# Kernel optimization log

Measured on AMD Instinct MI355X. Metric: run time of the kernel, lower is better.

Reference implementation:

```python
import jax, jax.numpy as jnp
import numpy as np

RANGE_EXTENDER = 5.0
EPS = 1e-8  # torch cosine_similarity eps

N_CLASSES = 256
LATENT = 256
H = W = 256


def setup_inputs() -> dict:
    key = jax.random.key(0)
    k1, k2, k3 = jax.random.split(key, 3)
    x = jax.random.normal(k1, (LATENT, H, W), dtype=jnp.float32)
    weights = jax.random.normal(k2, (N_CLASSES, LATENT), dtype=jnp.float32)
    scale = jax.random.normal(k3, (N_CLASSES,), dtype=jnp.float32)
    return {"x": x, "weights": weights, "scale": scale}


def reference(x, weights, scale):
    # out[c,i,j] = cos_sim(x[:,i,j], weights[c]) * scale[c] * RANGE_EXTENDER
    x_norm = jnp.sqrt(jnp.sum(x * x, axis=0, keepdims=True))           # (1, H, W)
    xn = x / jnp.maximum(x_norm, EPS)                                   # (D, H, W)
    w_norm = jnp.sqrt(jnp.sum(weights * weights, axis=1, keepdims=True))  # (C, 1)
    wn = weights / jnp.maximum(w_norm, EPS)                             # (C, D)
    cos = jnp.einsum("cd,dhw->chw", wn, xn)                            # (C, H, W)
    return cos * scale[:, None, None] * RANGE_EXTENDER
```

## Files before the change

kernel.cpp:

```cpp
#include <hip/hip_runtime.h>
#include <stdint.h>

typedef unsigned short u16;
typedef __bf16 bf16_t;
typedef bf16_t bf16x8 __attribute__((ext_vector_type(8)));
typedef float f32x4 __attribute__((ext_vector_type(4)));

static constexpr int P = 65536;

__device__ __forceinline__ float bfbits2f(uint32_t b) {
    union { uint32_t i; float f; } u; u.i = b << 16; return u.f;
}
__device__ __forceinline__ u16 f2bf(float f) {
    union { float f; uint32_t i; } u; u.f = f;
    uint32_t x = u.i + 0x7FFFu + ((u.i >> 16) & 1u);
    return (u16)(x >> 16);
}
__device__ __forceinline__ uint32_t pack2(float a, float b) {
    return (uint32_t)f2bf(a) | ((uint32_t)f2bf(b) << 16);
}

__device__ __forceinline__ int detect_bf16_input(const void* Xg) {
    const uint32_t* Xu = (const uint32_t*)Xg;
    const int lane = (int)(threadIdx.x & 63);
    const uint32_t v = Xu[(size_t)lane * 131071u];
    const uint32_t e = (v >> 7) & 0xFFu;
    unsigned long long m = __ballot(e >= 96u && e <= 135u);
    return __popcll(m) >= 40;
}

__global__ __launch_bounds__(64) void coshead_prep(
    const void* __restrict__ Xg, const void* __restrict__ Wg,
    const void* __restrict__ Sg, float* __restrict__ rs_ws,
    u16* __restrict__ wbf)
{
    const int c    = (int)blockIdx.x;
    const int lane = (int)threadIdx.x;
    const int bf   = detect_bf16_input(Xg);
    float s;
    uint2 packed;
    if (bf) {
        const uint2 v = *(const uint2*)((const u16*)Wg + (size_t)c * 256 + lane * 4);
        const float a = bfbits2f(v.x & 0xFFFFu), b = bfbits2f(v.x >> 16);
        const float d = bfbits2f(v.y & 0xFFFFu), e = bfbits2f(v.y >> 16);
        s = a * a + b * b + d * d + e * e;
        packed = v;
    } else {
        const f32x4 v = *(const f32x4*)((const float*)Wg + (size_t)c * 256 + lane * 4);
        s = v[0] * v[0] + v[1] * v[1] + v[2] * v[2] + v[3] * v[3];
        packed.x = pack2(v[0], v[1]);
        packed.y = pack2(v[2], v[3]);
    }
    *(uint2*)(wbf + (size_t)c * 256 + lane * 4) = packed;
    s += __shfl_xor(s, 1);  s += __shfl_xor(s, 2);  s += __shfl_xor(s, 4);
    s += __shfl_xor(s, 8);  s += __shfl_xor(s, 16); s += __shfl_xor(s, 32);
    if (lane == 0) {
        const float sc = bf ? bfbits2f((uint32_t)((const u16*)Sg)[c])
                            : ((const float*)Sg)[c];
        rs_ws[c] = sc * 5.0f / fmaxf(sqrtf(s), 1e-8f);
    }
}

__global__ __launch_bounds__(256, 3) void coshead_gemm(
    const void* __restrict__ Xg_, const u16* __restrict__ Wbf,
    const float* __restrict__ rs_ws, float* __restrict__ Og)
{
    __shared__ char smem_[32768 + 8192];
    char* sA = smem_;
    char* sB = smem_ + 32768;

    const int t  = (int)threadIdx.x;
    const int l  = t & 63;
    const int w  = t >> 6;
    const int p0 = (int)blockIdx.x * 64;
    const int bf = detect_bf16_input(Xg_);

    const int g    = t & 7;
    const int r    = t >> 3;
    const int m16  = l & 15;
    const int quad = l >> 4;

    const int lrow = l >> 3;
    const int gsl  = (l & 7) ^ lrow;
    const u16* wsrc = Wbf + ((size_t)(w * 8 + lrow) << 8) + gsl * 8;
    char* ldsA = sA + w * 1024;

    float ssq[8];
#pragma unroll
    for (int j = 0; j < 8; ++j) ssq[j] = 0.f;
    f32x4 acc[4][4];
#pragma unroll
    for (int a = 0; a < 4; ++a)
#pragma unroll
        for (int b = 0; b < 4; ++b)
#pragma unroll
            for (int i = 0; i < 4; ++i) acc[a][b][i] = 0.f;

    f32x4 rA, rB, rC, rD;
    if (!bf) {
        const float* xp = (const float*)Xg_ + (size_t)(2 * r) * P + p0 + g * 8;
        rA = *(const f32x4*)xp;
        rB = *(const f32x4*)(xp + 4);
        rC = *(const f32x4*)(xp + P);
        rD = *(const f32x4*)(xp + P + 4);
    }

    for (int kc = 0; kc < 4; ++kc) {
#pragma unroll
        for (int j = 0; j < 8; ++j) {
            __builtin_amdgcn_global_load_lds(
                (const __attribute__((address_space(1))) void*)(wsrc + j * 8192 + kc * 64),
                (__attribute__((address_space(3))) void*)(ldsA + j * 4096),
                16, 0, 0);
        }

        if (bf) {
            const u16* xp = (const u16*)Xg_ + (size_t)(2 * r + kc * 64) * P + p0 + g * 8;
            const uint4 v0 = *(const uint4*)xp;
            const uint4 v1 = *(const uint4*)(xp + P);
            const uint32_t e0[4] = {v0.x, v0.y, v0.z, v0.w};
            const uint32_t e1[4] = {v1.x, v1.y, v1.z, v1.w};
#pragma unroll
            for (int d = 0; d < 4; ++d) {
                const float f00 = bfbits2f(e0[d] & 0xFFFFu), f01 = bfbits2f(e0[d] >> 16);
                const float f10 = bfbits2f(e1[d] & 0xFFFFu), f11 = bfbits2f(e1[d] >> 16);
                ssq[2 * d]     += f00 * f00 + f10 * f10;
                ssq[2 * d + 1] += f01 * f01 + f11 * f11;
                const uint32_t d0 = (e0[d] & 0xFFFFu) | (e1[d] << 16);
                const uint32_t d1 = (e0[d] >> 16) | (e1[d] & 0xFFFF0000u);
                const int pj0 = g * 8 + 2 * d, pj1 = pj0 + 1;
                *(uint32_t*)(sB + pj0 * 128 + (((r >> 2) ^ (pj0 & 7) ^ g) * 16) + (r & 3) * 4) = d0;
                *(uint32_t*)(sB + pj1 * 128 + (((r >> 2) ^ (pj1 & 7) ^ g) * 16) + (r & 3) * 4) = d1;
            }
        } else {
            const float f0[8] = {rA[0], rA[1], rA[2], rA[3], rB[0], rB[1], rB[2], rB[3]};
            const float f1[8] = {rC[0], rC[1], rC[2], rC[3], rD[0], rD[1], rD[2], rD[3]};
#pragma unroll
            for (int j = 0; j < 8; ++j) {
                ssq[j] += f0[j] * f0[j] + f1[j] * f1[j];
                const int pix = g * 8 + j;
                *(uint32_t*)(sB + pix * 128 + (((r >> 2) ^ (pix & 7) ^ g) * 16) + (r & 3) * 4) =
                    pack2(f0[j], f1[j]);
            }
        }
        __syncthreads();

        if (!bf && kc < 3) {
            const float* xp = (const float*)Xg_ + (size_t)(2 * r + (kc + 1) * 64) * P + p0 + g * 8;
            rA = *(const f32x4*)xp;
            rB = *(const f32x4*)(xp + 4);
            rC = *(const f32x4*)(xp + P);
            rD = *(const f32x4*)(xp + P + 4);
        }

#pragma unroll
        for (int kk = 0; kk < 2; ++kk) {
            bf16x8 af[4], bfr[4];
#pragma unroll
            for (int tm = 0; tm < 4; ++tm) {
                const int row = w * 64 + tm * 16 + m16;
                af[tm] = *(const bf16x8*)(sA + row * 128 + (((kk * 4 + quad) ^ (row & 7)) * 16));
            }
#pragma unroll
            for (int tn = 0; tn < 4; ++tn) {
                const int pix = tn * 16 + m16;
                bfr[tn] = *(const bf16x8*)(sB + pix * 128 +
                           (((kk * 4 + quad) ^ (pix & 7) ^ (pix >> 3)) * 16));
            }
#pragma unroll
            for (int tm = 0; tm < 4; ++tm)
#pragma unroll
                for (int tn = 0; tn < 4; ++tn)
                    acc[tm][tn] = __builtin_amdgcn_mfma_f32_16x16x32_bf16(
                        af[tm], bfr[tn], acc[tm][tn], 0, 0, 0);
        }
        __syncthreads();
    }

    float* xs   = (float*)sA;
    float* xinv = (float*)sB;
#pragma unroll
    for (int j = 0; j < 8; ++j) xs[r * 64 + g * 8 + j] = ssq[j];
    __syncthreads();
    if (t < 64) {
        float sx = 0.f;
#pragma unroll
        for (int rr = 0; rr < 32; ++rr) sx += xs[rr * 64 + t];
        xinv[t] = 1.0f / fmaxf(sqrtf(sx), 1e-8f);
    }
    __syncthreads();

    float inv4[4];
#pragma unroll
    for (int tn = 0; tn < 4; ++tn) inv4[tn] = xinv[tn * 16 + m16];
#pragma unroll
    for (int tm = 0; tm < 4; ++tm) {
        const int cbase = w * 64 + tm * 16 + quad * 4;
        const f32x4 rs4 = *(const f32x4*)(rs_ws + cbase);
#pragma unroll
        for (int tn = 0; tn < 4; ++tn) {
#pragma unroll
            for (int i = 0; i < 4; ++i) {
                Og[(size_t)(cbase + i) * P + p0 + tn * 16 + m16] =
                    acc[tm][tn][i] * rs4[i] * inv4[tn];
            }
        }
    }
}

extern "C" void kernel_launch(void* const* d_in, const int* in_sizes, int n_in,
                              void* d_out, int out_size, void* d_ws, size_t ws_size,
                              hipStream_t stream) {
    (void)out_size; (void)ws_size;
    const void* X = d_in[0];
    const void* W = d_in[1];
    const void* S = d_in[2];
    for (int i = 0; i < n_in; ++i) {
        if (in_sizes[i] == 256 * 65536) X = d_in[i];
        else if (in_sizes[i] == 256 * 256) W = d_in[i];
        else if (in_sizes[i] == 256)      S = d_in[i];
    }
    float* rs  = (float*)d_ws;
    u16*   wbf = (u16*)((char*)d_ws + 1024);
    coshead_prep<<<dim3(256), dim3(64), 0, stream>>>(X, W, S, rs, wbf);
    coshead_gemm<<<dim3(1024), dim3(256), 0, stream>>>(X, wbf, rs, (float*)d_out);
}
```

Measured before the change: 139.6 us.

## Keep full weight matrix resident in LDS and loop four pixel tiles per block

The GEMM kernel now loads the whole bf16 weight matrix (128 KB) into LDS once per block and reuses it across four 64-pixel tiles. The grid shrinks from 1024 to 256 blocks. The B tile is double-buffered, so one barrier per k-step replaces two, and the next X chunk is prefetched across tile boundaries. This cuts repeated weight traffic and per-block setup, at the cost of one block per CU (occupancy 1, launch bounds 256,1) with a 256-block grid, which may leave CUs idle or underused on a 256-CU part and loses latency hiding.

Result: faster. 131.6 us (-5.7%).

```diff
diff --git a/kernel.cpp b/kernel.cpp
--- a/kernel.cpp
+++ b/kernel.cpp
@@ -61,18 +61,19 @@
     }
 }
 
-__global__ __launch_bounds__(256, 3) void coshead_gemm(
+__global__ __launch_bounds__(256, 1) void coshead_gemm(
     const void* __restrict__ Xg_, const u16* __restrict__ Wbf,
     const float* __restrict__ rs_ws, float* __restrict__ Og)
 {
-    __shared__ char smem_[32768 + 8192];
-    char* sA = smem_;
-    char* sB = smem_ + 32768;
+    __shared__ char smem_[131072 + 16384 + 256];
+    char*  sA   = smem_;
+    char*  sB   = smem_ + 131072;
+    float* xinv = (float*)(smem_ + 131072 + 16384);
 
     const int t  = (int)threadIdx.x;
     const int l  = t & 63;
     const int w  = t >> 6;
-    const int p0 = (int)blockIdx.x * 64;
+    const int pbase = (int)blockIdx.x * 256;
     const int bf = detect_bf16_input(Xg_);
 
     const int g    = t & 7;
@@ -84,125 +85,152 @@
     const int gsl  = (l & 7) ^ lrow;
     const u16* wsrc = Wbf + ((size_t)(w * 8 + lrow) << 8) + gsl * 8;
     char* ldsA = sA + w * 1024;
-
-    float ssq[8];
-#pragma unroll
-    for (int j = 0; j < 8; ++j) ssq[j] = 0.f;
-    f32x4 acc[4][4];
-#pragma unroll
-    for (int a = 0; a < 4; ++a)
-#pragma unroll
-        for (int b = 0; b < 4; ++b)
-#pragma unroll
-            for (int i = 0; i < 4; ++i) acc[a][b][i] = 0.f;
+#pragma unroll
+    for (int j = 0; j < 8; ++j)
+#pragma unroll
+        for (int kc = 0; kc < 4; ++kc)
+            __builtin_amdgcn_global_load_lds(
+                (const __attribute__((address_space(1))) void*)(wsrc + j * 8192 + kc * 64),
+                (__attribute__((address_space(3))) void*)(ldsA + kc * 32768 + j * 4096),
+                16, 0, 0);
 
     f32x4 rA, rB, rC, rD;
-    if (!bf) {
-        const float* xp = (const float*)Xg_ + (size_t)(2 * r) * P + p0 + g * 8;
+    uint4 vb0, vb1;
+    if (bf) {
+        const u16* xp = (const u16*)Xg_ + (size_t)(2 * r) * P + pbase + g * 8;
+        vb0 = *(const uint4*)xp;
+        vb1 = *(const uint4*)(xp + P);
+    } else {
+        const float* xp = (const float*)Xg_ + (size_t)(2 * r) * P + pbase + g * 8;
         rA = *(const f32x4*)xp;
         rB = *(const f32x4*)(xp + 4);
         rC = *(const f32x4*)(xp + P);
         rD = *(const f32x4*)(xp + P + 4);
     }
 
-    for (int kc = 0; kc < 4; ++kc) {
-#pragma unroll
-        for (int j = 0; j < 8; ++j) {
-            __builtin_amdgcn_global_load_lds(
-                (const __attribute__((address_space(1))) void*)(wsrc + j * 8192 + kc * 64),
-                (__attribute__((address_space(3))) void*)(ldsA + j * 4096),
-                16, 0, 0);
+    for (int pt = 0; pt < 4; ++pt) {
+        const int p0 = pbase + pt * 64;
+
+        float ssq[8];
+#pragma unroll
+        for (int j = 0; j < 8; ++j) ssq[j] = 0.f;
+        f32x4 acc[4][4];
+#pragma unroll
+        for (int a = 0; a < 4; ++a)
+#pragma unroll
+            for (int b = 0; b < 4; ++b)
+#pragma unroll
+                for (int i = 0; i < 4; ++i) acc[a][b][i] = 0.f;
+
+        for (int kc = 0; kc < 4; ++kc) {
+            char* sBw = sB + (kc & 1) * 8192;
+
+            if (bf) {
+                const uint32_t e0[4] = {vb0.x, vb0.y, vb0.z, vb0.w};
+                const uint32_t e1[4] = {vb1.x, vb1.y, vb1.z, vb1.w};
+#pragma unroll
+                for (int d = 0; d < 4; ++d) {
+                    const float f00 = bfbits2f(e0[d] & 0xFFFFu), f01 = bfbits2f(e0[d] >> 16);
+                    const float f10 = bfbits2f(e1[d] & 0xFFFFu), f11 = bfbits2f(e1[d] >> 16);
+                    ssq[2 * d]     += f00 * f00 + f10 * f10;
+                    ssq[2 * d + 1] += f01 * f01 + f11 * f11;
+                    const uint32_t d0 = (e0[d] & 0xFFFFu) | (e1[d] << 16);
+                    const uint32_t d1 = (e0[d] >> 16) | (e1[d] & 0xFFFF0000u);
+                    const int pj0 = g * 8 + 2 * d, pj1 = pj0 + 1;
+                    *(uint32_t*)(sBw + pj0 * 128 + (((r >> 2) ^ (pj0 & 7) ^ g) * 16) + (r & 3) * 4) = d0;
+                    *(uint32_t*)(sBw + pj1 * 128 + (((r >> 2) ^ (pj1 & 7) ^ g) * 16) + (r & 3) * 4) = d1;
+                }
+            } else {
+                const float f0[8] = {rA[0], rA[1], rA[2], rA[3], rB[0], rB[1], rB[2], rB[3]};
+                const float f1[8] = {rC[0], rC[1], rC[2], rC[3], rD[0], rD[1], rD[2], rD[3]};
+#pragma unroll
+                for (int j = 0; j < 8; ++j) {
+                    ssq[j] += f0[j] * f0[j] + f1[j] * f1[j];
+                    const int pix = g * 8 + j;
+                    *(uint32_t*)(sBw + pix * 128 + (((r >> 2) ^ (pix & 7) ^ g) * 16) + (r & 3) * 4) =
+                        pack2(f0[j], f1[j]);
+                }
+            }
+
+            const int it = pt * 4 + kc;
+            if (it < 15) {
+                const int nk = (it + 1) & 3, np = (it + 1) >> 2;
+                if (bf) {
+                    const u16* xp = (const u16*)Xg_ + (size_t)(2 * r + nk * 64) * P
+                                    + pbase + np * 64 + g * 8;
+                    vb0 = *(const uint4*)xp;
+                    vb1 = *(const uint4*)(xp + P);
+                } else {
+                    const float* xp = (const float*)Xg_ + (size_t)(2 * r + nk * 64) * P
+                                      + pbase + np * 64 + g * 8;
+                    rA = *(const f32x4*)xp;
+                    rB = *(const f32x4*)(xp + 4);
+                    rC = *(const f32x4*)(xp + P);
+                    rD = *(const f32x4*)(xp + P + 4);
+                }
+            }
+
+            asm volatile("s_waitcnt lgkmcnt(0)" ::: "memory");
+            __builtin_amdgcn_sched_barrier(0);
+            __builtin_amdgcn_s_barrier();
+
+            const char* sAk = sA + kc * 32768;
+#pragma unroll
+            for (int kk = 0; kk < 2; ++kk) {
+                bf16x8 af[4], bfr[4];
+#pragma unroll
+                for (int tm = 0; tm < 4; ++tm) {
+                    const int row = w * 64 + tm * 16 + m16;
+                    af[tm] = *(const bf16x8*)(sAk + row * 128 + (((kk * 4 + quad) ^ (row & 7)) * 16));
+                }
+#pragma unroll
+                for (int tn = 0; tn < 4; ++tn) {
+                    const int pix = tn * 16 + m16;
+                    bfr[tn] = *(const bf16x8*)(sBw + pix * 128 +
+                               (((kk * 4 + quad) ^ (pix & 7) ^ (pix >> 3)) * 16));
+                }
+#pragma unroll
+                for (int tm = 0; tm < 4; ++tm)
+#pragma unroll
+                    for (int tn = 0; tn < 4; ++tn)
+                        acc[tm][tn] = __builtin_amdgcn_mfma_f32_16x16x32_bf16(
+                            af[tm], bfr[tn], acc[tm][tn], 0, 0, 0);
+            }
         }
 
-        if (bf) {
-            const u16* xp = (const u16*)Xg_ + (size_t)(2 * r + kc * 64) * P + p0 + g * 8;
-            const uint4 v0 = *(const uint4*)xp;
-            const uint4 v1 = *(const uint4*)(xp + P);
-            const uint32_t e0[4] = {v0.x, v0.y, v0.z, v0.w};
-            const uint32_t e1[4] = {v1.x, v1.y, v1.z, v1.w};
-#pragma unroll
-            for (int d = 0; d < 4; ++d) {
-                const float f00 = bfbits2f(e0[d] & 0xFFFFu), f01 = bfbits2f(e0[d] >> 16);
-                const float f10 = bfbits2f(e1[d] & 0xFFFFu), f11 = bfbits2f(e1[d] >> 16);
-                ssq[2 * d]     += f00 * f00 + f10 * f10;
-                ssq[2 * d + 1] += f01 * f01 + f11 * f11;
-                const uint32_t d0 = (e0[d] & 0xFFFFu) | (e1[d] << 16);
-                const uint32_t d1 = (e0[d] >> 16) | (e1[d] & 0xFFFF0000u);
-                const int pj0 = g * 8 + 2 * d, pj1 = pj0 + 1;
-                *(uint32_t*)(sB + pj0 * 128 + (((r >> 2) ^ (pj0 & 7) ^ g) * 16) + (r & 3) * 4) = d0;
-                *(uint32_t*)(sB + pj1 * 128 + (((r >> 2) ^ (pj1 & 7) ^ g) * 16) + (r & 3) * 4) = d1;
-            }
-        } else {
-            const float f0[8] = {rA[0], rA[1], rA[2], rA[3], rB[0], rB[1], rB[2], rB[3]};
-            const float f1[8] = {rC[0], rC[1], rC[2], rC[3], rD[0], rD[1], rD[2], rD[3]};
-#pragma unroll
-            for (int j = 0; j < 8; ++j) {
-                ssq[j] += f0[j] * f0[j] + f1[j] * f1[j];
-                const int pix = g * 8 + j;
-                *(uint32_t*)(sB + pix * 128 + (((r >> 2) ^ (pix & 7) ^ g) * 16) + (r & 3) * 4) =
-                    pack2(f0[j], f1[j]);
-            }
+        float* xs = (float*)(sB + 8192);
+        asm volatile("s_waitcnt lgkmcnt(0)" ::: "memory");
+        __builtin_amdgcn_sched_barrier(0);
+        __builtin_amdgcn_s_barrier();
+#pragma unroll
+        for (int j = 0; j < 8; ++j) xs[r * 64 + g * 8 + j] = ssq[j];
+        asm volatile("s_waitcnt lgkmcnt(0)" ::: "memory");
+        __builtin_amdgcn_sched_barrier(0);
+        __builtin_amdgcn_s_barrier();
+        if (t < 64) {
+            float sx = 0.f;
+#pragma unroll
+            for (int rr = 0; rr < 32; ++rr) sx += xs[rr * 64 + t];
+            xinv[t] = 1.0f / fmaxf(sqrtf(sx), 1e-8f);
         }
-        __syncthreads();
-
-        if (!bf && kc < 3) {
-            const float* xp = (const float*)Xg_ + (size_t)(2 * r + (kc + 1) * 64) * P + p0 + g * 8;
-            rA = *(const f32x4*)xp;
-            rB = *(const f32x4*)(xp + 4);
-            rC = *(const f32x4*)(xp + P);
-            rD = *(const f32x4*)(xp + P + 4);
-        }
-
-#pragma unroll
-        for (int kk = 0; kk < 2; ++kk) {
-            bf16x8 af[4], bfr[4];
-#pragma unroll
-            for (int tm = 0; tm < 4; ++tm) {
-                const int row = w * 64 + tm * 16 + m16;
-                af[tm] = *(const bf16x8*)(sA + row * 128 + (((kk * 4 + quad) ^ (row & 7)) * 16));
-            }
+        asm volatile("s_waitcnt lgkmcnt(0)" ::: "memory");
+        __builtin_amdgcn_sched_barrier(0);
+        __builtin_amdgcn_s_barrier();
+
+        float inv4[4];
+#pragma unroll
+        for (int tn = 0; tn < 4; ++tn) inv4[tn] = xinv[tn * 16 + m16];
+#pragma unroll
+        for (int tm = 0; tm < 4; ++tm) {
+            const int cbase = w * 64 + tm * 16 + quad * 4;
+            const f32x4 rs4 = *(const f32x4*)(rs_ws + cbase);
 #pragma unroll
             for (int tn = 0; tn < 4; ++tn) {
-                const int pix = tn * 16 + m16;
-                bfr[tn] = *(const bf16x8*)(sB + pix * 128 +
-                           (((kk * 4 + quad) ^ (pix & 7) ^ (pix >> 3)) * 16));
-            }
-#pragma unroll
-            for (int tm = 0; tm < 4; ++tm)
-#pragma unroll
-                for (int tn = 0; tn < 4; ++tn)
-                    acc[tm][tn] = __builtin_amdgcn_mfma_f32_16x16x32_bf16(
-                        af[tm], bfr[tn], acc[tm][tn], 0, 0, 0);
-        }
-        __syncthreads();
-    }
-
-    float* xs   = (float*)sA;
-    float* xinv = (float*)sB;
-#pragma unroll
-    for (int j = 0; j < 8; ++j) xs[r * 64 + g * 8 + j] = ssq[j];
-    __syncthreads();
-    if (t < 64) {
-        float sx = 0.f;
-#pragma unroll
-        for (int rr = 0; rr < 32; ++rr) sx += xs[rr * 64 + t];
-        xinv[t] = 1.0f / fmaxf(sqrtf(sx), 1e-8f);
-    }
-    __syncthreads();
-
-    float inv4[4];
-#pragma unroll
-    for (int tn = 0; tn < 4; ++tn) inv4[tn] = xinv[tn * 16 + m16];
-#pragma unroll
-    for (int tm = 0; tm < 4; ++tm) {
-        const int cbase = w * 64 + tm * 16 + quad * 4;
-        const f32x4 rs4 = *(const f32x4*)(rs_ws + cbase);
-#pragma unroll
-        for (int tn = 0; tn < 4; ++tn) {
-#pragma unroll
-            for (int i = 0; i < 4; ++i) {
-                Og[(size_t)(cbase + i) * P + p0 + tn * 16 + m16] =
-                    acc[tm][tn][i] * rs4[i] * inv4[tn];
+#pragma unroll
+                for (int i = 0; i < 4; ++i) {
+                    Og[(size_t)(cbase + i) * P + p0 + tn * 16 + m16] =
+                        acc[tm][tn][i] * rs4[i] * inv4[tn];
+                }
             }
         }
     }
@@ -223,5 +251,5 @@
     float* rs  = (float*)d_ws;
     u16*   wbf = (u16*)((char*)d_ws + 1024);
     coshead_prep<<<dim3(256), dim3(64), 0, stream>>>(X, W, S, rs, wbf);
-    coshead_gemm<<<dim3(1024), dim3(256), 0, stream>>>(X, wbf, rs, (float*)d_out);
-}
+    coshead_gemm<<<dim3(256), dim3(256), 0, stream>>>(X, wbf, rs, (float*)d_out);
+}
```
